# Kernel optimization log

Measured on AMD Instinct MI355X. Metric: run time of the kernel, lower is better.

## Reference

```python
import jax, jax.numpy as jnp
from jax import lax
import numpy as np

D_MODEL = 1024
D_STATE = 16
D_CONV = 4
EXPAND = 2
D_INNER = EXPAND * D_MODEL          # 2048
DT_RANK = D_MODEL // 16             # 64 (mamba 'auto' dt_rank)
B, L = 1, 1024


def setup_inputs() -> dict:
    key = jax.random.key(0)
    ks = jax.random.split(key, 8)

    def nrm(k, shape, s=0.02):
        return jax.random.normal(k, shape, jnp.float32) * s

    def mamba_params(kbase):
        k = jax.random.split(kbase, 7)
        return {
            'in_w': nrm(k[0], (2 * D_INNER, D_MODEL)),            # in_proj (no bias)
            'conv_w': nrm(k[1], (D_INNER, 1, D_CONV), 0.1),       # depthwise causal conv
            'conv_b': nrm(k[2], (D_INNER,), 0.1),
            'xproj_w': nrm(k[3], (DT_RANK + 2 * D_STATE, D_INNER)),
            'dt_w': nrm(k[4], (D_INNER, DT_RANK), 0.1),
            'dt_b': nrm(k[5], (D_INNER,), 0.1),
            'Alog': jnp.log(jnp.broadcast_to(jnp.arange(1., D_STATE + 1, dtype=jnp.float32), (D_INNER, D_STATE))),
            'Dp': jnp.ones((D_INNER,), jnp.float32),
            'out_w': nrm(k[6], (D_MODEL, D_INNER)),
        }

    fw = mamba_params(ks[0])
    bw = mamba_params(ks[1])
    inp = {'x': jax.random.normal(ks[2], (B, L, D_MODEL), jnp.float32)}
    for n, p in fw.items():
        inp['fw_' + n] = p
    for n, p in bw.items():
        inp['bw_' + n] = p
    inp['proj_w'] = nrm(ks[3], (D_MODEL, 2 * D_MODEL))
    inp['proj_b'] = jnp.zeros((D_MODEL,), jnp.float32)
    inp['ln_w'] = jnp.ones((D_MODEL,), jnp.float32)
    inp['ln_b'] = jnp.zeros((D_MODEL,), jnp.float32)
    return inp


def _mamba(x, in_w, conv_w, conv_b, xproj_w, dt_w, dt_b, Alog, Dp, out_w):
    # x: [B, L, d_model]
    xz = x @ in_w.T                                    # [B, L, 2*d_inner]
    xi, z = jnp.split(xz, 2, axis=-1)
    # causal depthwise conv over time
    xc = lax.conv_general_dilated(jnp.swapaxes(xi, 1, 2), conv_w, (1,),
                                  [(D_CONV - 1, 0)], feature_group_count=D_INNER)
    u = jnp.swapaxes(jax.nn.silu(xc + conv_b[None, :, None]), 1, 2)   # [B, L, d_inner]
    x_dbl = u @ xproj_w.T                              # [B, L, dt_rank + 2*d_state]
    dt = x_dbl[..., :DT_RANK]
    Bm = x_dbl[..., DT_RANK:DT_RANK + D_STATE]
    Cm = x_dbl[..., DT_RANK + D_STATE:]
    delta = jax.nn.softplus(dt @ dt_w.T + dt_b)        # [B, L, d_inner]
    A = -jnp.exp(Alog)                                 # [d_inner, d_state]
    dA = jnp.exp(jnp.einsum('bld,dn->bldn', delta, A))
    dBu = jnp.einsum('bld,bln,bld->bldn', delta, Bm, u)

    def step(h, inputs):
        a, b, c = inputs                               # a,b: [B,D,N]; c: [B,N]
        h = a * h + b
        return h, jnp.einsum('bdn,bn->bd', h, c)

    h0 = jnp.zeros((x.shape[0], D_INNER, D_STATE), x.dtype)
    _, ys = lax.scan(step, h0, (jnp.moveaxis(dA, 1, 0), jnp.moveaxis(dBu, 1, 0), jnp.moveaxis(Cm, 1, 0)))
    y = jnp.moveaxis(ys, 0, 1) + u * Dp                # [B, L, d_inner]
    return (y * jax.nn.silu(z)) @ out_w.T              # [B, L, d_model]


def _block(x,
           fw_in_w, fw_conv_w, fw_conv_b, fw_xproj_w, fw_dt_w, fw_dt_b, fw_Alog, fw_Dp, fw_out_w,
           bw_in_w, bw_conv_w, bw_conv_b, bw_xproj_w, bw_dt_w, bw_dt_b, bw_Alog, bw_Dp, bw_out_w,
           proj_w, proj_b, ln_w, ln_b):
    out_fw = _mamba(x, fw_in_w, fw_conv_w, fw_conv_b, fw_xproj_w, fw_dt_w, fw_dt_b, fw_Alog, fw_Dp, fw_out_w) + x
    xb = jnp.flip(x, axis=1)
    out_bw = jnp.flip(_mamba(xb, bw_in_w, bw_conv_w, bw_conv_b, bw_xproj_w, bw_dt_w, bw_dt_b, bw_Alog, bw_Dp, bw_out_w) + xb, axis=1)
    out = jnp.concatenate([out_fw, out_bw], axis=-1) @ proj_w.T + proj_b
    mu = out.mean(-1, keepdims=True)
    var = out.var(-1, keepdims=True)
    return (out - mu) / jnp.sqrt(var + 1e-5) * ln_w + ln_b


def reference(x,
              fw_in_w, fw_conv_w, fw_conv_b, fw_xproj_w, fw_dt_w, fw_dt_b, fw_Alog, fw_Dp, fw_out_w,
              bw_in_w, bw_conv_w, bw_conv_b, bw_xproj_w, bw_dt_w, bw_dt_b, bw_Alog, bw_Dp, bw_out_w,
              proj_w, proj_b, ln_w, ln_b):
    return _block(x,
                  fw_in_w, fw_conv_w, fw_conv_b, fw_xproj_w, fw_dt_w, fw_dt_b, fw_Alog, fw_Dp, fw_out_w,
                  bw_in_w, bw_conv_w, bw_conv_b, bw_xproj_w, bw_dt_w, bw_dt_b, bw_Alog, bw_Dp, bw_out_w,
                  proj_w, proj_b, ln_w, ln_b)
```

## Files before the change

kernel.cpp:

```cpp
#include <hip/hip_runtime.h>

typedef __bf16 bf16;
typedef __bf16 bf16x8 __attribute__((ext_vector_type(8)));
typedef float  f32x4  __attribute__((ext_vector_type(4)));

#define L_SEQ 1024
#define DM    1024
#define DI    2048
#define DTR   64
#define DSTATE 16
#define XD    96
#define NC    64
#define CS    16

__device__ __forceinline__ float bf2f(bf16 v){ return (float)v; }
__device__ __forceinline__ bf16  f2bf(float v){ return (bf16)v; }

__device__ __forceinline__ void gl_lds16(const bf16* g, bf16* l) {
  __builtin_amdgcn_global_load_lds(
      (const __attribute__((address_space(1))) unsigned int*)g,
      (__attribute__((address_space(3))) unsigned int*)l, 16, 0, 0);
}

#define OFF_X      0L
#define OFF_INW    1048576L
#define OFF_XPROJ  9437184L
#define OFF_DTW    9830400L
#define OFF_OUTW   10092544L
#define OFF_PROJW  14286848L
#define CVT_TOTAL  16384000L

__global__ __launch_bounds__(256) void cvt_k(
    const float* __restrict__ x,
    const float* __restrict__ inw0, const float* __restrict__ inw1,
    const float* __restrict__ xp0,  const float* __restrict__ xp1,
    const float* __restrict__ dt0,  const float* __restrict__ dt1,
    const float* __restrict__ ow0,  const float* __restrict__ ow1,
    const float* __restrict__ pw,   bf16* __restrict__ wb)
{
  long i = ((long)blockIdx.x * 256 + threadIdx.x) * 8;
  if (i >= CVT_TOTAL) return;
  const float* src; long off;
  if      (i < OFF_INW)                 { src = x;    off = i - OFF_X; }
  else if (i < OFF_INW + 4194304L)      { src = inw0; off = i - OFF_INW; }
  else if (i < OFF_XPROJ)               { src = inw1; off = i - (OFF_INW + 4194304L); }
  else if (i < OFF_XPROJ + 196608L)     { src = xp0;  off = i - OFF_XPROJ; }
  else if (i < OFF_DTW)                 { src = xp1;  off = i - (OFF_XPROJ + 196608L); }
  else if (i < OFF_DTW + 131072L)       { src = dt0;  off = i - OFF_DTW; }
  else if (i < OFF_OUTW)                { src = dt1;  off = i - (OFF_DTW + 131072L); }
  else if (i < OFF_OUTW + 2097152L)     { src = ow0;  off = i - OFF_OUTW; }
  else if (i < OFF_PROJW)               { src = ow1;  off = i - (OFF_OUTW + 2097152L); }
  else                                  { src = pw;   off = i - OFF_PROJW; }
  f32x4 v0 = *(const f32x4*)(src + off);
  f32x4 v1 = *(const f32x4*)(src + off + 4);
  bf16x8 t;
  #pragma unroll
  for (int q = 0; q < 4; q++) { t[q] = (bf16)v0[q]; t[4+q] = (bf16)v1[q]; }
  *(bf16x8*)(wb + i) = t;
}

template<int BM, int BN>
__global__ __launch_bounds__(256) void gemm_bt(
    const bf16* __restrict__ A, const bf16* __restrict__ B0, const bf16* __restrict__ B1,
    void* __restrict__ Cv,
    int M, int N, int K, int lda, int ldb, int ldc,
    long aOffZ, long cOffZ,
    const float* __restrict__ bias0, const float* __restrict__ bias1,
    int flipA1, int writeBf16, int act,
    const float* __restrict__ xF, int fuseRes)
{
  constexpr int WM = BM / 2, WN = BN / 2;
  constexpr int MI = WM / 16, NJ = WN / 16;
  constexpr int ACALLS = BM / 32;
  constexpr int BCALLS = BN / 32;

  const int tid  = threadIdx.x;
  const int z    = blockIdx.z;
  const bf16*  Bp   = z ? B1 : B0;
  const float* bias = z ? bias1 : bias0;
  const int flip = z ? flipA1 : 0;
  const int bm = blockIdx.x * BM;
  const int bn = blockIdx.y * BN;

  __shared__ bf16 As[BM * 64];
  __shared__ bf16 Bs[BN * 64];

  f32x4 acc[MI][NJ];
  #pragma unroll
  for (int i=0;i<MI;i++)
    #pragma unroll
    for (int j=0;j<NJ;j++) { acc[i][j][0]=0.f; acc[i][j][1]=0.f; acc[i][j][2]=0.f; acc[i][j][3]=0.f; }

  const int wave = tid >> 6;
  const int lane = tid & 63;
  const int wm = (wave >> 1) * WM;
  const int wn = (wave & 1) * WN;
  const int fr  = lane & 15;
  const int frx = fr & 7;
  const int kqc = lane >> 4;

  const bf16* aSrc[ACALLS];
  int aOff[ACALLS];
  #pragma unroll
  for (int t = 0; t < ACALLS; t++) {
    int s = (wave * ACALLS + t) * 64 + lane;
    int r = s >> 3;
    int j = (s & 7) ^ (r & 7);
    int ar = bm + r;
    int agr = flip ? (M - 1 - ar) : ar;
    aSrc[t] = A + (long)z * aOffZ + (long)agr * lda + j * 8;
    aOff[t] = (wave * ACALLS + t) * 512;
  }
  const bf16* bSrc[BCALLS];
  int bOff[BCALLS];
  #pragma unroll
  for (int t = 0; t < BCALLS; t++) {
    int s = (wave * BCALLS + t) * 64 + lane;
    int r = s >> 3;
    int j = (s & 7) ^ (r & 7);
    int br = bn + r; if (br > N - 1) br = N - 1;
    bSrc[t] = Bp + (long)br * ldb + j * 8;
    bOff[t] = (wave * BCALLS + t) * 512;
  }

  for (int k0 = 0; k0 < K; k0 += 64) {
    #pragma unroll
    for (int t = 0; t < ACALLS; t++) gl_lds16(aSrc[t] + k0, &As[aOff[t]]);
    #pragma unroll
    for (int t = 0; t < BCALLS; t++) gl_lds16(bSrc[t] + k0, &Bs[bOff[t]]);
    __syncthreads();

    #pragma unroll
    for (int ks8 = 0; ks8 < 8; ks8 += 4) {
      bf16x8 af[MI], bfr[NJ];
      #pragma unroll
      for (int i=0;i<MI;i++) {
        int row = wm + i*16 + fr;
        af[i]  = *(const bf16x8*)&As[(row * 8 + ((ks8 + kqc) ^ frx)) * 8];
      }
      #pragma unroll
      for (int j=0;j<NJ;j++) {
        int row = wn + j*16 + fr;
        bfr[j] = *(const bf16x8*)&Bs[(row * 8 + ((ks8 + kqc) ^ frx)) * 8];
      }
      #pragma unroll
      for (int i=0;i<MI;i++)
        #pragma unroll
        for (int j=0;j<NJ;j++)
          acc[i][j] = __builtin_amdgcn_mfma_f32_16x16x32_bf16(af[i], bfr[j], acc[i][j], 0, 0, 0);
    }
    __syncthreads();
  }

  const int rr = (lane >> 4) * 4;
  const int cc = lane & 15;
  #pragma unroll
  for (int i=0;i<MI;i++) {
    #pragma unroll
    for (int j=0;j<NJ;j++) {
      int gn = bn + wn + j*16 + cc;
      if (gn >= N) continue;
      float bv = bias ? bias[gn] : 0.f;
      #pragma unroll
      for (int r=0;r<4;r++) {
        int gm = bm + wm + i*16 + rr + r;
        float v = acc[i][j][r] + bv;
        if (fuseRes) {
          long row = z ? (long)(M - 1 - gm) : (long)gm;
          float o = v + xF[row * DM + gn];
          ((bf16*)Cv)[row * (2 * DM) + (long)z * DM + gn] = f2bf(o);
        } else {
          if (act == 1) v = (v > 20.f) ? v : log1pf(__expf(v));
          long idx = (long)z * cOffZ + (long)gm * ldc + gn;
          if (writeBf16) ((bf16*)Cv)[idx] = f2bf(v);
          else           ((float*)Cv)[idx] = v;
        }
      }
    }
  }
}

__global__ __launch_bounds__(256) void conv_silu_k(
    const bf16* __restrict__ xz, const float* __restrict__ cw0, const float* __restrict__ cw1,
    const float* __restrict__ cb0, const float* __restrict__ cb1, bf16* __restrict__ u)
{
  int gid = blockIdx.x * 256 + threadIdx.x;
  int dir = gid >> 18;
  int rem = gid & ((1 << 18) - 1);
  int l = rem >> 8;
  int d0 = (rem & 255) * 8;
  const float* w = dir ? cw1 : cw0;
  const float* b = dir ? cb1 : cb0;
  const bf16* xzd = xz + (long)dir * L_SEQ * (2 * DI);
  float acc[8];
  #pragma unroll
  for (int q = 0; q < 8; q++) acc[q] = b[d0 + q];
  #pragma unroll
  for (int j = 0; j < 4; j++) {
    int ll = l - 3 + j;
    if (ll < 0) continue;
    bf16x8 xv = *(const bf16x8*)(xzd + (long)ll * (2 * DI) + d0);
    #pragma unroll
    for (int q = 0; q < 8; q++) acc[q] += w[(d0 + q) * 4 + j] * bf2f(xv[q]);
  }
  bf16x8 o;
  #pragma unroll
  for (int q = 0; q < 8; q++) {
    float s = acc[q] / (1.f + __expf(-acc[q]));
    o[q] = f2bf(s);
  }
  *(bf16x8*)(u + (long)dir * L_SEQ * DI + (long)l * DI + d0) = o;
}

__global__ __launch_bounds__(256) void scan_p1(
    const bf16* __restrict__ xz, const bf16* __restrict__ u, const bf16* __restrict__ xdbl,
    const float* __restrict__ Alog0, const float* __restrict__ Alog1,
    bf16* __restrict__ hout, float* __restrict__ sumd)
{
  const int tid = threadIdx.x;
  const int c   = blockIdx.y;
  const int dir = blockIdx.z;
  const int d   = blockIdx.x * 256 + tid;
  const float* Alog = dir ? Alog1 : Alog0;
  const bf16* dl = xz + (long)dir * L_SEQ * (2 * DI);
  const bf16* ud = u  + (long)dir * L_SEQ * DI;
  const bf16* xd = xdbl + (long)dir * L_SEQ * XD;
  const int l0 = c * CS;

  __shared__ float lb[CS][16];
  {
    int ll = tid >> 4, n = tid & 15;
    lb[ll][n] = bf2f(xd[(long)(l0 + ll) * XD + DTR + n]);
  }

  float dl_r[CS], uu_r[CS];
  #pragma unroll
  for (int s = 0; s < CS; s++) {
    dl_r[s] = bf2f(dl[(long)(l0 + s) * (2 * DI) + d]);
    uu_r[s] = bf2f(ud[(long)(l0 + s) * DI + d]);
  }
  __syncthreads();

  float An[16], h[16];
  #pragma unroll
  for (int n = 0; n < 16; n++) { An[n] = -__expf(Alog[d * 16 + n]); h[n] = 0.f; }
  float sd = 0.f;

  #pragma unroll
  for (int ll = 0; ll < CS; ll++) {
    float dlt = dl_r[ll];
    sd += dlt;
    float du = dlt * uu_r[ll];
    #pragma unroll
    for (int n = 0; n < 16; n++) {
      float a = __expf(dlt * An[n]);
      h[n] = h[n] * a + du * lb[ll][n];
    }
  }

  bf16* hp = hout + (((long)dir * NC + c) * DI + d) * 16;
  bf16x8 o0, o1;
  #pragma unroll
  for (int n = 0; n < 8; n++) { o0[n] = f2bf(h[n]); o1[n] = f2bf(h[8 + n]); }
  *(bf16x8*)hp = o0;
  *(bf16x8*)(hp + 8) = o1;
  sumd[((long)dir * NC + c) * DI + d] = sd;
}

__global__ __launch_bounds__(256) void scan_p2(
    const float* __restrict__ Alog0, const float* __restrict__ Alog1,
    bf16* hout, const float* __restrict__ sumd)
{
  int g = blockIdx.x * 256 + threadIdx.x;
  int dir = g >> 15;
  int rem = g & 32767;
  int d = rem >> 4;
  int n = rem & 15;
  const float* Alog = dir ? Alog1 : Alog0;
  float An = -__expf(Alog[d * 16 + n]);
  float hs = 0.f;
  #pragma unroll 4
  for (int c = 0; c < NC; c++) {
    long base = ((long)dir * NC + c) * DI + d;
    float tmp = bf2f(hout[base * 16 + n]);
    float P = __expf(An * sumd[base]);
    hout[base * 16 + n] = f2bf(hs);
    hs = P * hs + tmp;
  }
}

__global__ __launch_bounds__(256) void scan_p3(
    const bf16* xz, const bf16* u, const bf16* __restrict__ xdbl,
    const float* __restrict__ Alog0, const float* __restrict__ Alog1,
    const float* __restrict__ Dp0, const float* __restrict__ Dp1,
    const bf16* __restrict__ hout, bf16* g)
{
  const int tid = threadIdx.x;
  const int c   = blockIdx.y;
  const int dir = blockIdx.z;
  const int d   = blockIdx.x * 256 + tid;
  const float* Alog = dir ? Alog1 : Alog0;
  const float* Dp   = dir ? Dp1 : Dp0;
  const bf16* row0 = xz + (long)dir * L_SEQ * (2 * DI);
  const bf16* ud   = u  + (long)dir * L_SEQ * DI;
  const bf16* xd   = xdbl + (long)dir * L_SEQ * XD;
  bf16* gd = g + (long)dir * L_SEQ * DI;
  const int l0 = c * CS;

  __shared__ float lb[CS][16];
  __shared__ float lc[CS][16];
  {
    int i = tid * 2;
    int ll = i >> 5, j = i & 31;
    const bf16* p = xd + (long)(l0 + ll) * XD + DTR + j;
    float v0 = bf2f(p[0]), v1 = bf2f(p[1]);
    if (j < 16) { lb[ll][j] = v0; lb[ll][j + 1] = v1; }
    else        { lc[ll][j - 16] = v0; lc[ll][j - 15] = v1; }
  }

  float dl_r[CS], uu_r[CS], zv_r[CS];
  #pragma unroll
  for (int s = 0; s < CS; s++) {
    dl_r[s] = bf2f(row0[(long)(l0 + s) * (2 * DI) + d]);
    zv_r[s] = bf2f(row0[(long)(l0 + s) * (2 * DI) + DI + d]);
    uu_r[s] = bf2f(ud[(long)(l0 + s) * DI + d]);
  }
  const bf16* hp = hout + (((long)dir * NC + c) * DI + d) * 16;
  bf16x8 h0 = *(const bf16x8*)hp;
  bf16x8 h1 = *(const bf16x8*)(hp + 8);
  __syncthreads();

  float An[16], h[16];
  #pragma unroll
  for (int n = 0; n < 16; n++) {
    An[n] = -__expf(Alog[d * 16 + n]);
    h[n] = bf2f(n < 8 ? h0[n & 7] : h1[n & 7]);
  }
  const float Dpv = Dp[d];

  #pragma unroll
  for (int ll = 0; ll < CS; ll++) {
    float dlt = dl_r[ll];
    float du = dlt * uu_r[ll];
    float y = 0.f;
    #pragma unroll
    for (int n = 0; n < 16; n++) {
      float a = __expf(dlt * An[n]);
      h[n] = h[n] * a + du * lb[ll][n];
      y += h[n] * lc[ll][n];
    }
    y += uu_r[ll] * Dpv;
    float zv = zv_r[ll];
    float sz = zv / (1.f + __expf(-zv));
    gd[(long)(l0 + ll) * DI + d] = f2bf(y * sz);
  }
}

__global__ __launch_bounds__(256) void ln_k(
    const float* __restrict__ fin, const float* __restrict__ pb,
    const float* __restrict__ lnw, const float* __restrict__ lnb, float* __restrict__ out)
{
  int row = blockIdx.x;
  int tid = threadIdx.x;
  float v[4]; float s1 = 0.f, s2 = 0.f;
  #pragma unroll
  for (int j = 0; j < 4; j++) {
    int c = tid + j * 256;
    v[j] = fin[(long)row * DM + c] + pb[c];
    s1 += v[j]; s2 += v[j] * v[j];
  }
  #pragma unroll
  for (int off = 32; off; off >>= 1) { s1 += __shfl_down(s1, off); s2 += __shfl_down(s2, off); }
  __shared__ float red[8];
  int wave = tid >> 6, lane = tid & 63;
  if (lane == 0) { red[wave] = s1; red[4 + wave] = s2; }
  __syncthreads();
  float t1 = red[0] + red[1] + red[2] + red[3];
  float t2 = red[4] + red[5] + red[6] + red[7];
  float mu = t1 / DM;
  float var = t2 / DM - mu * mu;
  float inv = rsqrtf(var + 1e-5f);
  #pragma unroll
  for (int j = 0; j < 4; j++) {
    int c = tid + j * 256;
    out[(long)row * DM + c] = (v[j] - mu) * inv * lnw[c] + lnb[c];
  }
}

extern "C" void kernel_launch(void* const* d_in, const int* in_sizes, int n_in,
                              void* d_out, int out_size, void* d_ws, size_t ws_size,
                              hipStream_t stream)
{
  const float* x         = (const float*)d_in[0];
  const float* fw_conv_w = (const float*)d_in[2];
  const float* fw_conv_b = (const float*)d_in[3];
  const float* fw_dt_b   = (const float*)d_in[6];
  const float* fw_Alog   = (const float*)d_in[7];
  const float* fw_Dp     = (const float*)d_in[8];
  const float* bw_conv_w = (const float*)d_in[11];
  const float* bw_conv_b = (const float*)d_in[12];
  const float* bw_dt_b   = (const float*)d_in[15];
  const float* bw_Alog   = (const float*)d_in[16];
  const float* bw_Dp     = (const float*)d_in[17];
  const float* proj_b    = (const float*)d_in[20];
  const float* ln_w      = (const float*)d_in[21];
  const float* ln_b      = (const float*)d_in[22];

  char* ws = (char*)d_ws;
  const size_t MB = 1024 * 1024;
  bf16*  xz    = (bf16*)(ws + 0);
  bf16*  u     = (bf16*)(ws + 16 * MB);
  bf16*  xdbl  = (bf16*)(ws + 24 * MB);
  float* sumd  = (float*)(ws + 25 * MB);
  bf16*  hout  = (bf16*)(ws + 26 * MB);
  bf16*  wb    = (bf16*)(ws + 34 * MB);
  bf16*  g     = u;
  bf16*  delta = xz;
  bf16*  fused = (bf16*)(ws + 0);
  float* fin   = (float*)(ws + 4 * MB);

  bf16* xb     = wb + OFF_X;
  bf16* inw    = wb + OFF_INW;
  bf16* xprojw = wb + OFF_XPROJ;
  bf16* dtw    = wb + OFF_DTW;
  bf16* outw   = wb + OFF_OUTW;
  bf16* projw  = wb + OFF_PROJW;

  dim3 blk(256);

  cvt_k<<<(CVT_TOTAL / 8 + 255) / 256, blk, 0, stream>>>(
      x, (const float*)d_in[1], (const float*)d_in[10],
      (const float*)d_in[4], (const float*)d_in[13],
      (const float*)d_in[5], (const float*)d_in[14],
      (const float*)d_in[9], (const float*)d_in[18],
      (const float*)d_in[19], wb);

  gemm_bt<64,128><<<dim3(16, 32, 2), blk, 0, stream>>>(
      xb, inw, inw + 4194304L, (void*)xz, 1024, 4096, 1024, 1024, 1024, 4096,
      0L, (long)1024 * 4096, nullptr, nullptr, 1, 1, 0, nullptr, 0);

  conv_silu_k<<<2048, blk, 0, stream>>>(xz, fw_conv_w, bw_conv_w, fw_conv_b, bw_conv_b, u);

  gemm_bt<32,64><<<dim3(32, 2, 2), blk, 0, stream>>>(
      u, xprojw, xprojw + 196608L, (void*)xdbl, 1024, 96, 2048, 2048, 2048, 96,
      (long)1024 * 2048, (long)1024 * 96, nullptr, nullptr, 0, 1, 0, nullptr, 0);

  gemm_bt<64,128><<<dim3(16, 16, 2), blk, 0, stream>>>(
      xdbl, dtw, dtw + 131072L, (void*)delta, 1024, 2048, 64, 96, 64, 4096,
      (long)1024 * 96, (long)1024 * 4096, fw_dt_b, bw_dt_b, 0, 1, 1, nullptr, 0);

  scan_p1<<<dim3(8, NC, 2), blk, 0, stream>>>(xz, u, xdbl, fw_Alog, bw_Alog, hout, sumd);
  scan_p2<<<dim3(256), blk, 0, stream>>>(fw_Alog, bw_Alog, hout, sumd);
  scan_p3<<<dim3(8, NC, 2), blk, 0, stream>>>(xz, u, xdbl, fw_Alog, bw_Alog,
                                              fw_Dp, bw_Dp, hout, g);

  gemm_bt<32,64><<<dim3(32, 16, 2), blk, 0, stream>>>(
      g, outw, outw + 2097152L, (void*)fused, 1024, 1024, 2048, 2048, 2048, 1024,
      (long)1024 * 2048, 0L, nullptr, nullptr, 0, 1, 0, x, 1);

  gemm_bt<32,64><<<dim3(32, 16, 1), blk, 0, stream>>>(
      fused, projw, projw, (void*)fin, 1024, 1024, 2048, 2048, 2048, 1024,
      0L, 0L, nullptr, nullptr, 0, 0, 0, nullptr, 0);

  ln_k<<<1024, blk, 0, stream>>>(fin, proj_b, ln_w, ln_b, (float*)d_out);
}
```

Baseline: 336.4 us.

## Split in_proj output into separate x and z buffers with contiguous rows

The in_proj GEMM epilogue now writes the x half and the z half into two separate buffers with row stride DI, instead of one interleaved 2*DI-stride array. The conv, scan_p1 and scan_p3 kernels read the compact buffers, and the delta GEMM writes delta into the x buffer at the compact stride using smaller tiles (32x64). Softplus is rewritten as a stable max plus log form using fast intrinsics. The aim is denser memory access and better occupancy for the small-K delta GEMM, at the cost of one extra branch per element in the GEMM epilogue.

```diff
diff --git a/kernel.cpp b/kernel.cpp
--- a/kernel.cpp
+++ b/kernel.cpp
@@ -62,7 +62,7 @@
 template<int BM, int BN>
 __global__ __launch_bounds__(256) void gemm_bt(
     const bf16* __restrict__ A, const bf16* __restrict__ B0, const bf16* __restrict__ B1,
-    void* __restrict__ Cv,
+    void* __restrict__ Cv, void* __restrict__ Cv2, int splitN,
     int M, int N, int K, int lda, int ldb, int ldc,
     long aOffZ, long cOffZ,
     const float* __restrict__ bias0, const float* __restrict__ bias1,
@@ -170,10 +170,13 @@
           float o = v + xF[row * DM + gn];
           ((bf16*)Cv)[row * (2 * DM) + (long)z * DM + gn] = f2bf(o);
         } else {
-          if (act == 1) v = (v > 20.f) ? v : log1pf(__expf(v));
-          long idx = (long)z * cOffZ + (long)gm * ldc + gn;
-          if (writeBf16) ((bf16*)Cv)[idx] = f2bf(v);
-          else           ((float*)Cv)[idx] = v;
+          if (act == 1) v = fmaxf(v, 0.f) + __logf(1.f + __expf(-fabsf(v)));
+          int gn2 = gn;
+          void* Cp = Cv;
+          if (gn >= splitN) { gn2 = gn - splitN; Cp = Cv2; }
+          long idx = (long)z * cOffZ + (long)gm * ldc + gn2;
+          if (writeBf16) ((bf16*)Cp)[idx] = f2bf(v);
+          else           ((float*)Cp)[idx] = v;
         }
       }
     }
@@ -181,7 +184,7 @@
 }
 
 __global__ __launch_bounds__(256) void conv_silu_k(
-    const bf16* __restrict__ xz, const float* __restrict__ cw0, const float* __restrict__ cw1,
+    const bf16* __restrict__ xi, const float* __restrict__ cw0, const float* __restrict__ cw1,
     const float* __restrict__ cb0, const float* __restrict__ cb1, bf16* __restrict__ u)
 {
   int gid = blockIdx.x * 256 + threadIdx.x;
@@ -191,7 +194,7 @@
   int d0 = (rem & 255) * 8;
   const float* w = dir ? cw1 : cw0;
   const float* b = dir ? cb1 : cb0;
-  const bf16* xzd = xz + (long)dir * L_SEQ * (2 * DI);
+  const bf16* xid = xi + (long)dir * L_SEQ * DI;
   float acc[8];
   #pragma unroll
   for (int q = 0; q < 8; q++) acc[q] = b[d0 + q];
@@ -199,7 +202,7 @@
   for (int j = 0; j < 4; j++) {
     int ll = l - 3 + j;
     if (ll < 0) continue;
-    bf16x8 xv = *(const bf16x8*)(xzd + (long)ll * (2 * DI) + d0);
+    bf16x8 xv = *(const bf16x8*)(xid + (long)ll * DI + d0);
     #pragma unroll
     for (int q = 0; q < 8; q++) acc[q] += w[(d0 + q) * 4 + j] * bf2f(xv[q]);
   }
@@ -213,7 +216,7 @@
 }
 
 __global__ __launch_bounds__(256) void scan_p1(
-    const bf16* __restrict__ xz, const bf16* __restrict__ u, const bf16* __restrict__ xdbl,
+    const bf16* __restrict__ delta, const bf16* __restrict__ u, const bf16* __restrict__ xdbl,
     const float* __restrict__ Alog0, const float* __restrict__ Alog1,
     bf16* __restrict__ hout, float* __restrict__ sumd)
 {
@@ -222,9 +225,9 @@
   const int dir = blockIdx.z;
   const int d   = blockIdx.x * 256 + tid;
   const float* Alog = dir ? Alog1 : Alog0;
-  const bf16* dl = xz + (long)dir * L_SEQ * (2 * DI);
-  const bf16* ud = u  + (long)dir * L_SEQ * DI;
-  const bf16* xd = xdbl + (long)dir * L_SEQ * XD;
+  const bf16* dl = delta + (long)dir * L_SEQ * DI;
+  const bf16* ud = u     + (long)dir * L_SEQ * DI;
+  const bf16* xd = xdbl  + (long)dir * L_SEQ * XD;
   const int l0 = c * CS;
 
   __shared__ float lb[CS][16];
@@ -236,7 +239,7 @@
   float dl_r[CS], uu_r[CS];
   #pragma unroll
   for (int s = 0; s < CS; s++) {
-    dl_r[s] = bf2f(dl[(long)(l0 + s) * (2 * DI) + d]);
+    dl_r[s] = bf2f(dl[(long)(l0 + s) * DI + d]);
     uu_r[s] = bf2f(ud[(long)(l0 + s) * DI + d]);
   }
   __syncthreads();
@@ -290,7 +293,7 @@
 }
 
 __global__ __launch_bounds__(256) void scan_p3(
-    const bf16* xz, const bf16* u, const bf16* __restrict__ xdbl,
+    const bf16* delta, const bf16* zb, const bf16* u, const bf16* __restrict__ xdbl,
     const float* __restrict__ Alog0, const float* __restrict__ Alog1,
     const float* __restrict__ Dp0, const float* __restrict__ Dp1,
     const bf16* __restrict__ hout, bf16* g)
@@ -301,9 +304,10 @@
   const int d   = blockIdx.x * 256 + tid;
   const float* Alog = dir ? Alog1 : Alog0;
   const float* Dp   = dir ? Dp1 : Dp0;
-  const bf16* row0 = xz + (long)dir * L_SEQ * (2 * DI);
-  const bf16* ud   = u  + (long)dir * L_SEQ * DI;
-  const bf16* xd   = xdbl + (long)dir * L_SEQ * XD;
+  const bf16* dl = delta + (long)dir * L_SEQ * DI;
+  const bf16* zd = zb    + (long)dir * L_SEQ * DI;
+  const bf16* ud = u     + (long)dir * L_SEQ * DI;
+  const bf16* xd = xdbl  + (long)dir * L_SEQ * XD;
   bf16* gd = g + (long)dir * L_SEQ * DI;
   const int l0 = c * CS;
 
@@ -321,8 +325,8 @@
   float dl_r[CS], uu_r[CS], zv_r[CS];
   #pragma unroll
   for (int s = 0; s < CS; s++) {
-    dl_r[s] = bf2f(row0[(long)(l0 + s) * (2 * DI) + d]);
-    zv_r[s] = bf2f(row0[(long)(l0 + s) * (2 * DI) + DI + d]);
+    dl_r[s] = bf2f(dl[(long)(l0 + s) * DI + d]);
+    zv_r[s] = bf2f(zd[(long)(l0 + s) * DI + d]);
     uu_r[s] = bf2f(ud[(long)(l0 + s) * DI + d]);
   }
   const bf16* hp = hout + (((long)dir * NC + c) * DI + d) * 16;
@@ -408,14 +412,15 @@
 
   char* ws = (char*)d_ws;
   const size_t MB = 1024 * 1024;
-  bf16*  xz    = (bf16*)(ws + 0);
+  bf16*  xi    = (bf16*)(ws + 0);
+  bf16*  zb    = (bf16*)(ws + 8 * MB);
   bf16*  u     = (bf16*)(ws + 16 * MB);
   bf16*  xdbl  = (bf16*)(ws + 24 * MB);
   float* sumd  = (float*)(ws + 25 * MB);
   bf16*  hout  = (bf16*)(ws + 26 * MB);
   bf16*  wb    = (bf16*)(ws + 34 * MB);
   bf16*  g     = u;
-  bf16*  delta = xz;
+  bf16*  delta = xi;
   bf16*  fused = (bf16*)(ws + 0);
   float* fin   = (float*)(ws + 4 * MB);
 
@@ -427,6 +432,7 @@
   bf16* projw  = wb + OFF_PROJW;
 
   dim3 blk(256);
+  const int BIGN = 1 << 30;
 
   cvt_k<<<(CVT_TOTAL / 8 + 255) / 256, blk, 0, stream>>>(
       x, (const float*)d_in[1], (const float*)d_in[10],
@@ -436,30 +442,35 @@
       (const float*)d_in[19], wb);
 
   gemm_bt<64,128><<<dim3(16, 32, 2), blk, 0, stream>>>(
-      xb, inw, inw + 4194304L, (void*)xz, 1024, 4096, 1024, 1024, 1024, 4096,
-      0L, (long)1024 * 4096, nullptr, nullptr, 1, 1, 0, nullptr, 0);
-
-  conv_silu_k<<<2048, blk, 0, stream>>>(xz, fw_conv_w, bw_conv_w, fw_conv_b, bw_conv_b, u);
+      xb, inw, inw + 4194304L, (void*)xi, (void*)zb, 2048,
+      1024, 4096, 1024, 1024, 1024, 2048,
+      0L, (long)1024 * 2048, nullptr, nullptr, 1, 1, 0, nullptr, 0);
+
+  conv_silu_k<<<2048, blk, 0, stream>>>(xi, fw_conv_w, bw_conv_w, fw_conv_b, bw_conv_b, u);
 
   gemm_bt<32,64><<<dim3(32, 2, 2), blk, 0, stream>>>(
-      u, xprojw, xprojw + 196608L, (void*)xdbl, 1024, 96, 2048, 2048, 2048, 96,
+      u, xprojw, xprojw + 196608L, (void*)xdbl, nullptr, BIGN,
+      1024, 96, 2048, 2048, 2048, 96,
       (long)1024 * 2048, (long)1024 * 96, nullptr, nullptr, 0, 1, 0, nullptr, 0);
 
-  gemm_bt<64,128><<<dim3(16, 16, 2), blk, 0, stream>>>(
-      xdbl, dtw, dtw + 131072L, (void*)delta, 1024, 2048, 64, 96, 64, 4096,
-      (long)1024 * 96, (long)1024 * 4096, fw_dt_b, bw_dt_b, 0, 1, 1, nullptr, 0);
-
-  scan_p1<<<dim3(8, NC, 2), blk, 0, stream>>>(xz, u, xdbl, fw_Alog, bw_Alog, hout, sumd);
+  gemm_bt<32,64><<<dim3(32, 32, 2), blk, 0, stream>>>(
+      xdbl, dtw, dtw + 131072L, (void*)delta, nullptr, BIGN,
+      1024, 2048, 64, 96, 64, 2048,
+      (long)1024 * 96, (long)1024 * 2048, fw_dt_b, bw_dt_b, 0, 1, 1, nullptr, 0);
+
+  scan_p1<<<dim3(8, NC, 2), blk, 0, stream>>>(delta, u, xdbl, fw_Alog, bw_Alog, hout, sumd);
   scan_p2<<<dim3(256), blk, 0, stream>>>(fw_Alog, bw_Alog, hout, sumd);
-  scan_p3<<<dim3(8, NC, 2), blk, 0, stream>>>(xz, u, xdbl, fw_Alog, bw_Alog,
+  scan_p3<<<dim3(8, NC, 2), blk, 0, stream>>>(delta, zb, u, xdbl, fw_Alog, bw_Alog,
                                               fw_Dp, bw_Dp, hout, g);
 
   gemm_bt<32,64><<<dim3(32, 16, 2), blk, 0, stream>>>(
-      g, outw, outw + 2097152L, (void*)fused, 1024, 1024, 2048, 2048, 2048, 1024,
+      g, outw, outw + 2097152L, (void*)fused, nullptr, BIGN,
+      1024, 1024, 2048, 2048, 2048, 1024,
       (long)1024 * 2048, 0L, nullptr, nullptr, 0, 1, 0, x, 1);
 
   gemm_bt<32,64><<<dim3(32, 16, 1), blk, 0, stream>>>(
-      fused, projw, projw, (void*)fin, 1024, 1024, 2048, 2048, 2048, 1024,
+      fused, projw, projw, (void*)fin, nullptr, BIGN,
+      1024, 1024, 2048, 2048, 2048, 1024,
       0L, 0L, nullptr, nullptr, 0, 0, 0, nullptr, 0);
 
   ln_k<<<1024, blk, 0, stream>>>(fin, proj_b, ln_w, ln_b, (float*)d_out);
```

Measured after the change: 324.3 us. 3.6% less time.
